# Optimization experiments

Hardware: AMD Instinct MI355X
Metric: run time of the kernel (lower is better)

The kernel has to match this reference:

```python
import jax, jax.numpy as jnp
import numpy as np

B, N, D, K = 1024, 8192, 256, 8
LAMBDA_MULT = 0.01

def setup_inputs() -> dict:
    key = jax.random.key(0)
    k1, k2, k3, k4, k5 = jax.random.split(key, 5)
    x = jax.random.uniform(k1, (B, D), dtype=jnp.float32)
    mu = jax.random.uniform(k2, (N, D), dtype=jnp.float32)
    lambda_base = jax.random.uniform(k3, (N,), dtype=jnp.float32) * LAMBDA_MULT
    v = jax.random.normal(k4, (N, K, D), dtype=jnp.float32)  # stands in for per-unit orthogonal init
    omega = 0.1 + 0.4 * jax.random.uniform(k5, (N, K), dtype=jnp.float32)
    return {"x": x, "mu": mu, "lambda_base": lambda_base, "v": v, "omega": omega}

def reference(x, mu, lambda_base, v, omega):
    # quad_form = diff^T (lambda*I + sum_k omega_k v_k v_k^T) diff
    #           = lambda * ||x - mu||^2 + sum_k omega_k * ((x - mu) . v_k)^2
    # Woodbury-style expansion avoids materializing W:(n,d,d) and diff:(b,n,d).
    x2 = jnp.sum(x * x, axis=-1)                      # (b,)
    mu2 = jnp.sum(mu * mu, axis=-1)                   # (n,)
    xm = x @ mu.T                                     # (b,n)
    sqdist = x2[:, None] - 2.0 * xm + mu2[None, :]    # (b,n) = ||x-mu||^2
    xv = jnp.einsum('bd,nkd->bnk', x, v)              # (b,n,k)
    muv = jnp.einsum('nd,nkd->nk', mu, v)             # (n,k)
    proj2 = (xv - muv[None, :, :]) ** 2               # (b,n,k)
    quad = lambda_base[None, :] * sqdist + jnp.einsum('bnk,nk->bn', proj2, omega)
    return jnp.exp(-quad / D)  # Type == 'exp'
```

## Files before the change

kernel.cpp:

```cpp
#include <hip/hip_runtime.h>


#define B_SZ 1024
#define N_SZ 8192
#define D_SZ 256
#define K_SZ 8

#define BTM 256
#define BT 128
#define NT 16

typedef __bf16 bf16x8 __attribute__((ext_vector_type(8)));
typedef float f32x4 __attribute__((ext_vector_type(4)));
typedef unsigned short u16x4 __attribute__((ext_vector_type(4)));
typedef unsigned short u16x8 __attribute__((ext_vector_type(8)));

#define WS_X2   0u
#define WS_MU2  4096u
#define WS_MUV  36864u
#define WS_PX   299008u
#define WS_PW   823296u
#define WS_NEED (823296ull + 37748736ull)

__device__ __forceinline__ float wave_reduce(float s) {
#pragma unroll
  for (int off = 32; off > 0; off >>= 1) s += __shfl_down(s, off);
  return s;
}

__device__ __forceinline__ u16x4 cvt4(float4 t) {
  u16x4 r;
  r[0] = __builtin_bit_cast(unsigned short, (__bf16)t.x);
  r[1] = __builtin_bit_cast(unsigned short, (__bf16)t.y);
  r[2] = __builtin_bit_cast(unsigned short, (__bf16)t.z);
  r[3] = __builtin_bit_cast(unsigned short, (__bf16)t.w);
  return r;
}

__device__ __forceinline__ void glds16(const void* g, const void* l) {
  __builtin_amdgcn_global_load_lds(
      (const __attribute__((address_space(1))) void*)g,
      (__attribute__((address_space(3))) void*)l, 16, 0, 0);
}

__global__ void prep_all(const float* __restrict__ x, const float* __restrict__ mu,
                         const float* __restrict__ v,
                         float* __restrict__ x2, unsigned short* __restrict__ px,
                         float* __restrict__ mu2, float* __restrict__ muv,
                         unsigned short* __restrict__ pw) {
  const int w = threadIdx.x >> 6, lane = threadIdx.x & 63;
  const int g = blockIdx.x * 4 + w;
  if (g < B_SZ) {
    const int b = g;
    float4 t = *(const float4*)(x + (size_t)b * D_SZ + 4 * lane);
    *(u16x4*)(px + (size_t)b * D_SZ + 4 * lane) = cvt4(t);
    float s = t.x * t.x + t.y * t.y + t.z * t.z + t.w * t.w;
    s = wave_reduce(s);
    if (lane == 0) x2[b] = s;
  } else if (g < B_SZ + N_SZ) {
    const int n = g - B_SZ;
    float4 m4 = *(const float4*)(mu + (size_t)n * D_SZ + 4 * lane);
    *(u16x4*)(pw + (size_t)n * 9 * D_SZ + 4 * lane) = cvt4(m4);
    float s = m4.x * m4.x + m4.y * m4.y + m4.z * m4.z + m4.w * m4.w;
    s = wave_reduce(s);
    if (lane == 0) mu2[n] = s;
  } else {
    const int idx = g - (B_SZ + N_SZ);
    const int n = idx >> 3, k = idx & 7;
    float4 m4 = *(const float4*)(mu + (size_t)n * D_SZ + 4 * lane);
    float4 v4 = *(const float4*)(v + ((size_t)n * K_SZ + k) * D_SZ + 4 * lane);
    *(u16x4*)(pw + ((size_t)n * 9 + k + 1) * D_SZ + 4 * lane) = cvt4(v4);
    float s = m4.x * v4.x + m4.y * v4.y + m4.z * v4.z + m4.w * v4.w;
    s = wave_reduce(s);
    if (lane == 0) muv[n * K_SZ + k] = s;
  }
}

__device__ __forceinline__ void stage_tile(const unsigned short* __restrict__ px,
                                           const unsigned short* __restrict__ pw,
                                           unsigned short* As, unsigned short* Bs,
                                           int b0, int n0, int k0, int w, int lane) {
  const int nl4 = lane >> 2;
  const int ch = lane & 3;
  const int kc = (ch ^ ((nl4 >> 1) & 3)) * 8;
#pragma unroll
  for (int t = 0; t < 4; ++t) {
    int r0 = w * 64 + t * 16;
    glds16(px + (size_t)(b0 + r0 + nl4) * D_SZ + k0 + kc, As + r0 * 32);
  }
#pragma unroll
  for (int t = 0; t < 3; ++t) {
    int i = w + 4 * t;
    if (i < 9)
      glds16(pw + ((size_t)(n0 + nl4) * 9 + i) * D_SZ + k0 + kc, Bs + i * 16 * 32);
  }
}

__global__ __launch_bounds__(256, 2)
void hmu_main_p(const unsigned short* __restrict__ px,
                const unsigned short* __restrict__ pw,
                const float* __restrict__ lam, const float* __restrict__ om,
                const float* __restrict__ wsf, float* __restrict__ out) {
  __shared__ __align__(16) unsigned short As[2][BTM * 32];
  __shared__ __align__(16) unsigned short Bs[2][NT * 9 * 32];

  const float* ws_x2 = wsf;
  const float* ws_mu2 = wsf + 1024;
  const float* ws_muv = wsf + 9216;

  const int tid = threadIdx.x;
  const int lane = tid & 63;
  const int w = tid >> 6;
  const int m = lane & 15;
  const int kg = lane >> 4;

  const int bid = blockIdx.x;
  const int xcd = bid & 7;
  const int idx = bid >> 3;
  const int n0 = (xcd * 64 + (idx >> 2)) * NT;
  const int b0 = (idx & 3) * BTM;

  f32x4 acc[4][9];
#pragma unroll
  for (int rb = 0; rb < 4; ++rb)
#pragma unroll
    for (int j = 0; j < 9; ++j) acc[rb][j] = (f32x4){0.f, 0.f, 0.f, 0.f};

  const int sw = (kg ^ ((m >> 1) & 3)) * 8;

  stage_tile(px, pw, As[0], Bs[0], b0, n0, 0, w, lane);

#pragma unroll
  for (int kt = 0; kt < 8; ++kt) {
    const int cur = kt & 1;
    if (kt < 7) {
      stage_tile(px, pw, As[cur ^ 1], Bs[cur ^ 1], b0, n0, (kt + 1) * 32, w, lane);
      if (w == 0) asm volatile("s_waitcnt vmcnt(7)" ::: "memory");
      else        asm volatile("s_waitcnt vmcnt(6)" ::: "memory");
    } else {
      asm volatile("s_waitcnt vmcnt(0)" ::: "memory");
    }
    __builtin_amdgcn_s_barrier();

    const unsigned short* Ac = As[cur];
    const unsigned short* Bc = Bs[cur];
    bf16x8 bfr[9];
#pragma unroll
    for (int j = 0; j < 9; ++j)
      bfr[j] = *(const bf16x8*)&Bc[(j * 16 + m) * 32 + sw];
    __builtin_amdgcn_s_setprio(1);
#pragma unroll
    for (int rb = 0; rb < 4; ++rb) {
      bf16x8 a = *(const bf16x8*)&Ac[((w * 4 + rb) * 16 + m) * 32 + sw];
#pragma unroll
      for (int j = 0; j < 9; ++j)
        acc[rb][j] = __builtin_amdgcn_mfma_f32_16x16x32_bf16(a, bfr[j], acc[rb][j], 0, 0, 0);
    }
    __builtin_amdgcn_s_setprio(0);
    if (kt < 7) {
      asm volatile("s_waitcnt lgkmcnt(0)" ::: "memory");
      __builtin_amdgcn_s_barrier();
    }
  }

  const int n = n0 + m;
  const float lam_n = lam[n];
  const float mu2_n = ws_mu2[n];
  float omr[8], muvr[8];
#pragma unroll
  for (int k = 0; k < 8; ++k) {
    omr[k] = om[n * 8 + k];
    muvr[k] = ws_muv[n * 8 + k];
  }
#pragma unroll
  for (int rb = 0; rb < 4; ++rb) {
#pragma unroll
    for (int r = 0; r < 4; ++r) {
      int b = b0 + (w * 4 + rb) * 16 + kg * 4 + r;
      float x2b = ws_x2[b];
      float c0 = acc[rb][0][r];
      float q = lam_n * (x2b - 2.f * c0 + mu2_n);
#pragma unroll
      for (int k = 0; k < 8; ++k) {
        float p = acc[rb][k + 1][r] - muvr[k];
        q = fmaf(omr[k] * p, p, q);
      }
      out[(size_t)b * N_SZ + n] = __expf(q * (-1.0f / 256.0f));
    }
  }
}

__device__ __forceinline__ void cvt16_store(const float* __restrict__ src,
                                            unsigned short* dst) {
  const float4* p4 = (const float4*)src;
  float fv[16];
#pragma unroll
  for (int e = 0; e < 4; ++e) {
    float4 t = p4[e];
    fv[4 * e + 0] = t.x; fv[4 * e + 1] = t.y;
    fv[4 * e + 2] = t.z; fv[4 * e + 3] = t.w;
  }
  u16x8 lo, hi;
#pragma unroll
  for (int e = 0; e < 8; ++e) {
    lo[e] = __builtin_bit_cast(unsigned short, (__bf16)fv[e]);
    hi[e] = __builtin_bit_cast(unsigned short, (__bf16)fv[e + 8]);
  }
  *(u16x8*)dst = lo;
  *(u16x8*)(dst + 8) = hi;
}

#define LDS_STRIDE 40
__global__ __launch_bounds__(256, 2)
void hmu_main_f(const float* __restrict__ x, const float* __restrict__ mu,
                const float* __restrict__ lam, const float* __restrict__ v,
                const float* __restrict__ om, const float* __restrict__ ws,
                float* __restrict__ out) {
  __shared__ __align__(16) unsigned short As[BT * LDS_STRIDE];
  __shared__ __align__(16) unsigned short Bs[NT * 9 * LDS_STRIDE];
  const float* ws_x2 = ws;
  const float* ws_mu2 = ws + 1024;
  const float* ws_muv = ws + 9216;
  const int tid = threadIdx.x, lane = tid & 63, w = tid >> 6;
  const int m = lane & 15, kg = lane >> 4;
  const int n0 = blockIdx.x * NT, b0 = blockIdx.y * BT;
  f32x4 acc[2][9];
#pragma unroll
  for (int bs = 0; bs < 2; ++bs)
#pragma unroll
    for (int j = 0; j < 9; ++j) acc[bs][j] = (f32x4){0.f, 0.f, 0.f, 0.f};
  const int arow = tid >> 1, ahalf = tid & 1;
  for (int kt = 0; kt < 8; ++kt) {
    const int k0 = kt * 32;
    cvt16_store(x + (size_t)(b0 + arow) * D_SZ + k0 + ahalf * 16,
                &As[arow * LDS_STRIDE + ahalf * 16]);
#pragma unroll
    for (int it = 0; it < 2; ++it) {
      int idx = tid + 256 * it;
      if (idx < 288) {
        int row = idx >> 1, half = idx & 1;
        int nl = row / 9, j = row - nl * 9;
        const float* src = (j == 0)
            ? mu + (size_t)(n0 + nl) * D_SZ + k0 + half * 16
            : v + (size_t)((n0 + nl) * K_SZ + (j - 1)) * D_SZ + k0 + half * 16;
        cvt16_store(src, &Bs[row * LDS_STRIDE + half * 16]);
      }
    }
    __syncthreads();
    bf16x8 af[2];
#pragma unroll
    for (int bs = 0; bs < 2; ++bs)
      af[bs] = *(const bf16x8*)&As[((2 * w + bs) * 16 + m) * LDS_STRIDE + kg * 8];
#pragma unroll
    for (int j = 0; j < 9; ++j) {
      bf16x8 bfr = *(const bf16x8*)&Bs[(m * 9 + j) * LDS_STRIDE + kg * 8];
      acc[0][j] = __builtin_amdgcn_mfma_f32_16x16x32_bf16(af[0], bfr, acc[0][j], 0, 0, 0);
      acc[1][j] = __builtin_amdgcn_mfma_f32_16x16x32_bf16(af[1], bfr, acc[1][j], 0, 0, 0);
    }
    __syncthreads();
  }
  const int n = n0 + m;
  const float lam_n = lam[n];
  const float mu2_n = ws_mu2[n];
  float omr[8], muvr[8];
#pragma unroll
  for (int k = 0; k < 8; ++k) {
    omr[k] = om[n * 8 + k];
    muvr[k] = ws_muv[n * 8 + k];
  }
#pragma unroll
  for (int bs = 0; bs < 2; ++bs)
#pragma unroll
    for (int r = 0; r < 4; ++r) {
      int b = b0 + (2 * w + bs) * 16 + kg * 4 + r;
      float c0 = acc[bs][0][r];
      float q = lam_n * (ws_x2[b] - 2.f * c0 + mu2_n);
#pragma unroll
      for (int k = 0; k < 8; ++k) {
        float p = acc[bs][k + 1][r] - muvr[k];
        q = fmaf(omr[k] * p, p, q);
      }
      out[(size_t)b * N_SZ + n] = __expf(q * (-1.0f / 256.0f));
    }
}

__global__ void p2_mu_f(const float* __restrict__ mu, const float* __restrict__ v,
                        float* __restrict__ mu2, float* __restrict__ muv) {
  __shared__ __align__(16) float mulds[D_SZ];
  const int n = blockIdx.x;
  const int w = threadIdx.x >> 6, lane = threadIdx.x & 63;
  if (w == 0) {
    float4 m4 = *(const float4*)(mu + (size_t)n * D_SZ + 4 * lane);
    *(float4*)(mulds + 4 * lane) = m4;
    float s = m4.x * m4.x + m4.y * m4.y + m4.z * m4.z + m4.w * m4.w;
    s = wave_reduce(s);
    if (lane == 0) mu2[n] = s;
  }
  __syncthreads();
  float4 m4 = *(const float4*)(mulds + 4 * lane);
#pragma unroll
  for (int kk = 0; kk < 2; ++kk) {
    const int k = w * 2 + kk;
    float4 v4 = *(const float4*)(v + ((size_t)n * K_SZ + k) * D_SZ + 4 * lane);
    float s = m4.x * v4.x + m4.y * v4.y + m4.z * v4.z + m4.w * v4.w;
    s = wave_reduce(s);
    if (lane == 0) muv[n * K_SZ + k] = s;
  }
}

__global__ void p1_x2_f(const float* __restrict__ x, float* __restrict__ x2) {
  const int w = threadIdx.x >> 6, lane = threadIdx.x & 63;
  const int b = blockIdx.x * 4 + w;
  float4 t = *(const float4*)(x + (size_t)b * D_SZ + 4 * lane);
  float s = t.x * t.x + t.y * t.y + t.z * t.z + t.w * t.w;
  s = wave_reduce(s);
  if (lane == 0) x2[b] = s;
}

extern "C" void kernel_launch(void* const* d_in, const int* in_sizes, int n_in,
                              void* d_out, int out_size, void* d_ws, size_t ws_size,
                              hipStream_t stream) {
  const float* x   = (const float*)d_in[0];
  const float* mu  = (const float*)d_in[1];
  const float* lam = (const float*)d_in[2];
  const float* v   = (const float*)d_in[3];
  const float* om  = (const float*)d_in[4];
  float* out = (float*)d_out;
  char* wsb = (char*)d_ws;
  float* wsf = (float*)d_ws;
  float* x2  = (float*)(wsb + WS_X2);
  float* mu2 = (float*)(wsb + WS_MU2);
  float* muv = (float*)(wsb + WS_MUV);

  if (ws_size >= WS_NEED) {
    unsigned short* px = (unsigned short*)(wsb + WS_PX);
    unsigned short* pw = (unsigned short*)(wsb + WS_PW);
    const int nunits = B_SZ + N_SZ + N_SZ * K_SZ;
    prep_all<<<nunits / 4, 256, 0, stream>>>(x, mu, v, x2, px, mu2, muv, pw);
    hmu_main_p<<<(N_SZ / NT) * (B_SZ / BTM), 256, 0, stream>>>(px, pw, lam, om, wsf, out);
  } else {
    dim3 grid(N_SZ / NT, B_SZ / BT);
    p1_x2_f<<<B_SZ / 4, 256, 0, stream>>>(x, x2);
    p2_mu_f<<<N_SZ, 256, 0, stream>>>(mu, v, mu2, muv);
    hmu_main_f<<<grid, 256, 0, stream>>>(x, mu, lam, v, om, wsf, out);
  }
}
```

Measured before the change: 161.6 us.

## Fuse mu/v bf16 conversion and mu2/muv reduction into main MFMA kernel

```diff
diff --git a/kernel.cpp b/kernel.cpp
--- a/kernel.cpp
+++ b/kernel.cpp
@@ -19,8 +19,7 @@
 #define WS_MU2  4096u
 #define WS_MUV  36864u
 #define WS_PX   299008u
-#define WS_PW   823296u
-#define WS_NEED (823296ull + 37748736ull)
+#define WS_NEED_FUSED (299008ull + 524288ull)
 
 __device__ __forceinline__ float wave_reduce(float s) {
 #pragma unroll
@@ -43,43 +42,20 @@
       (__attribute__((address_space(3))) void*)l, 16, 0, 0);
 }
 
-__global__ void prep_all(const float* __restrict__ x, const float* __restrict__ mu,
-                         const float* __restrict__ v,
-                         float* __restrict__ x2, unsigned short* __restrict__ px,
-                         float* __restrict__ mu2, float* __restrict__ muv,
-                         unsigned short* __restrict__ pw) {
+__global__ void prep_x(const float* __restrict__ x, float* __restrict__ x2,
+                       unsigned short* __restrict__ px) {
   const int w = threadIdx.x >> 6, lane = threadIdx.x & 63;
-  const int g = blockIdx.x * 4 + w;
-  if (g < B_SZ) {
-    const int b = g;
-    float4 t = *(const float4*)(x + (size_t)b * D_SZ + 4 * lane);
-    *(u16x4*)(px + (size_t)b * D_SZ + 4 * lane) = cvt4(t);
-    float s = t.x * t.x + t.y * t.y + t.z * t.z + t.w * t.w;
-    s = wave_reduce(s);
-    if (lane == 0) x2[b] = s;
-  } else if (g < B_SZ + N_SZ) {
-    const int n = g - B_SZ;
-    float4 m4 = *(const float4*)(mu + (size_t)n * D_SZ + 4 * lane);
-    *(u16x4*)(pw + (size_t)n * 9 * D_SZ + 4 * lane) = cvt4(m4);
-    float s = m4.x * m4.x + m4.y * m4.y + m4.z * m4.z + m4.w * m4.w;
-    s = wave_reduce(s);
-    if (lane == 0) mu2[n] = s;
-  } else {
-    const int idx = g - (B_SZ + N_SZ);
-    const int n = idx >> 3, k = idx & 7;
-    float4 m4 = *(const float4*)(mu + (size_t)n * D_SZ + 4 * lane);
-    float4 v4 = *(const float4*)(v + ((size_t)n * K_SZ + k) * D_SZ + 4 * lane);
-    *(u16x4*)(pw + ((size_t)n * 9 + k + 1) * D_SZ + 4 * lane) = cvt4(v4);
-    float s = m4.x * v4.x + m4.y * v4.y + m4.z * v4.z + m4.w * v4.w;
-    s = wave_reduce(s);
-    if (lane == 0) muv[n * K_SZ + k] = s;
-  }
-}
-
-__device__ __forceinline__ void stage_tile(const unsigned short* __restrict__ px,
-                                           const unsigned short* __restrict__ pw,
-                                           unsigned short* As, unsigned short* Bs,
-                                           int b0, int n0, int k0, int w, int lane) {
+  const int b = blockIdx.x * 4 + w;
+  float4 t = *(const float4*)(x + (size_t)b * D_SZ + 4 * lane);
+  *(u16x4*)(px + (size_t)b * D_SZ + 4 * lane) = cvt4(t);
+  float s = t.x * t.x + t.y * t.y + t.z * t.z + t.w * t.w;
+  s = wave_reduce(s);
+  if (lane == 0) x2[b] = s;
+}
+
+__device__ __forceinline__ void stage_A(const unsigned short* __restrict__ px,
+                                        unsigned short* As,
+                                        int b0, int k0, int w, int lane) {
   const int nl4 = lane >> 2;
   const int ch = lane & 3;
   const int kc = (ch ^ ((nl4 >> 1) & 3)) * 8;
@@ -88,25 +64,18 @@
     int r0 = w * 64 + t * 16;
     glds16(px + (size_t)(b0 + r0 + nl4) * D_SZ + k0 + kc, As + r0 * 32);
   }
-#pragma unroll
-  for (int t = 0; t < 3; ++t) {
-    int i = w + 4 * t;
-    if (i < 9)
-      glds16(pw + ((size_t)(n0 + nl4) * 9 + i) * D_SZ + k0 + kc, Bs + i * 16 * 32);
-  }
 }
 
 __global__ __launch_bounds__(256, 2)
-void hmu_main_p(const unsigned short* __restrict__ px,
-                const unsigned short* __restrict__ pw,
-                const float* __restrict__ lam, const float* __restrict__ om,
-                const float* __restrict__ wsf, float* __restrict__ out) {
+void hmu_fused(const unsigned short* __restrict__ px,
+               const float* __restrict__ mu, const float* __restrict__ v,
+               const float* __restrict__ lam, const float* __restrict__ om,
+               const float* __restrict__ wsf, float* __restrict__ out) {
+  __shared__ __align__(16) unsigned short Bs[8 * 144 * 32];
   __shared__ __align__(16) unsigned short As[2][BTM * 32];
-  __shared__ __align__(16) unsigned short Bs[2][NT * 9 * 32];
+  __shared__ float scr[16][10];
 
   const float* ws_x2 = wsf;
-  const float* ws_mu2 = wsf + 1024;
-  const float* ws_muv = wsf + 9216;
 
   const int tid = threadIdx.x;
   const int lane = tid & 63;
@@ -120,34 +89,56 @@
   const int n0 = (xcd * 64 + (idx >> 2)) * NT;
   const int b0 = (idx & 3) * BTM;
 
+  {
+    const int ktl = lane >> 3;
+    const int half = lane & 1;
+    const int c16 = (lane >> 1) & 3;
+#pragma unroll
+    for (int nn = 0; nn < 4; ++nn) {
+      const int nl = w * 4 + nn;
+      const int n = n0 + nl;
+      const int p = c16 ^ ((nl >> 1) & 3);
+      const int base = (ktl * 144 + nl) * 32 + p * 8 + half * 4;
+      float4 m4 = *(const float4*)(mu + (size_t)n * D_SZ + 4 * lane);
+      *(u16x4*)(Bs + base) = cvt4(m4);
+#pragma unroll
+      for (int j = 1; j <= 8; ++j) {
+        float4 v4 = *(const float4*)(v + ((size_t)n * K_SZ + (j - 1)) * D_SZ + 4 * lane);
+        *(u16x4*)(Bs + base + j * 16 * 32) = cvt4(v4);
+      }
+    }
+  }
+
+  stage_A(px, As[0], b0, 0, w, lane);
+  __syncthreads();
+
   f32x4 acc[4][9];
 #pragma unroll
   for (int rb = 0; rb < 4; ++rb)
 #pragma unroll
     for (int j = 0; j < 9; ++j) acc[rb][j] = (f32x4){0.f, 0.f, 0.f, 0.f};
+  f32x4 amu[3];
+#pragma unroll
+  for (int t = 0; t < 3; ++t) amu[t] = (f32x4){0.f, 0.f, 0.f, 0.f};
 
   const int sw = (kg ^ ((m >> 1) & 3)) * 8;
-
-  stage_tile(px, pw, As[0], Bs[0], b0, n0, 0, w, lane);
 
 #pragma unroll
   for (int kt = 0; kt < 8; ++kt) {
     const int cur = kt & 1;
     if (kt < 7) {
-      stage_tile(px, pw, As[cur ^ 1], Bs[cur ^ 1], b0, n0, (kt + 1) * 32, w, lane);
-      if (w == 0) asm volatile("s_waitcnt vmcnt(7)" ::: "memory");
-      else        asm volatile("s_waitcnt vmcnt(6)" ::: "memory");
+      stage_A(px, As[cur ^ 1], b0, (kt + 1) * 32, w, lane);
+      asm volatile("s_waitcnt vmcnt(4)" ::: "memory");
     } else {
       asm volatile("s_waitcnt vmcnt(0)" ::: "memory");
     }
     __builtin_amdgcn_s_barrier();
 
     const unsigned short* Ac = As[cur];
-    const unsigned short* Bc = Bs[cur];
     bf16x8 bfr[9];
 #pragma unroll
     for (int j = 0; j < 9; ++j)
-      bfr[j] = *(const bf16x8*)&Bc[(j * 16 + m) * 32 + sw];
+      bfr[j] = *(const bf16x8*)&Bs[(kt * 144 + j * 16 + m) * 32 + sw];
     __builtin_amdgcn_s_setprio(1);
 #pragma unroll
     for (int rb = 0; rb < 4; ++rb) {
@@ -155,6 +146,12 @@
 #pragma unroll
       for (int j = 0; j < 9; ++j)
         acc[rb][j] = __builtin_amdgcn_mfma_f32_16x16x32_bf16(a, bfr[j], acc[rb][j], 0, 0, 0);
+    }
+#pragma unroll
+    for (int t = 0; t < 3; ++t) {
+      const int jm = w + 4 * t;
+      if (jm < 9)
+        amu[t] = __builtin_amdgcn_mfma_f32_16x16x32_bf16(bfr[0], bfr[jm], amu[t], 0, 0, 0);
     }
     __builtin_amdgcn_s_setprio(0);
     if (kt < 7) {
@@ -163,14 +160,21 @@
     }
   }
 
+#pragma unroll
+  for (int t = 0; t < 3; ++t) {
+    const int jm = w + 4 * t;
+    if (jm < 9 && kg == (m >> 2)) scr[m][jm] = amu[t][m & 3];
+  }
+  __syncthreads();
+
   const int n = n0 + m;
   const float lam_n = lam[n];
-  const float mu2_n = ws_mu2[n];
+  const float mu2_n = scr[m][0];
   float omr[8], muvr[8];
 #pragma unroll
   for (int k = 0; k < 8; ++k) {
     omr[k] = om[n * 8 + k];
-    muvr[k] = ws_muv[n * 8 + k];
+    muvr[k] = scr[m][k + 1];
   }
 #pragma unroll
   for (int rb = 0; rb < 4; ++rb) {
@@ -329,16 +333,14 @@
   char* wsb = (char*)d_ws;
   float* wsf = (float*)d_ws;
   float* x2  = (float*)(wsb + WS_X2);
-  float* mu2 = (float*)(wsb + WS_MU2);
-  float* muv = (float*)(wsb + WS_MUV);
-
-  if (ws_size >= WS_NEED) {
+
+  if (ws_size >= WS_NEED_FUSED) {
     unsigned short* px = (unsigned short*)(wsb + WS_PX);
-    unsigned short* pw = (unsigned short*)(wsb + WS_PW);
-    const int nunits = B_SZ + N_SZ + N_SZ * K_SZ;
-    prep_all<<<nunits / 4, 256, 0, stream>>>(x, mu, v, x2, px, mu2, muv, pw);
-    hmu_main_p<<<(N_SZ / NT) * (B_SZ / BTM), 256, 0, stream>>>(px, pw, lam, om, wsf, out);
+    prep_x<<<B_SZ / 4, 256, 0, stream>>>(x, x2, px);
+    hmu_fused<<<(N_SZ / NT) * (B_SZ / BTM), 256, 0, stream>>>(px, mu, v, lam, om, wsf, out);
   } else {
+    float* mu2 = (float*)(wsb + WS_MU2);
+    float* muv = (float*)(wsb + WS_MUV);
     dim3 grid(N_SZ / NT, B_SZ / BT);
     p1_x2_f<<<B_SZ / 4, 256, 0, stream>>>(x, x2);
     p2_mu_f<<<N_SZ, 256, 0, stream>>>(mu, v, mu2, muv);
```

Measured after the change: 221.2 us. 1.37x slower.
